# Kernel tuning notes

Measured on AMD Instinct MI355X. Metric: run time of the kernel, lower is better.

## Reference

```python
import jax, jax.numpy as jnp
import numpy as np

B = 256
VERTS_PER_MESH = 5850
V = B * VERTS_PER_MESH
E = 3 * V
NEG_SLOPE = 0.01  # nn.LeakyReLU default


def setup_inputs() -> dict:
    key = jax.random.key(0)
    ks = jax.random.split(key, 10)
    inp = {
        "verts": jax.random.normal(ks[0], (V, 3), dtype=jnp.float32),
        "edges": jax.random.randint(ks[1], (E, 2), 0, V, dtype=jnp.int64)
        if jax.config.jax_enable_x64 else jax.random.randint(ks[1], (E, 2), 0, V, dtype=jnp.int32),
        # GraphConv 1: 3 -> 5 (pytorch3d init='normal': weights ~ N(0, 0.01), bias 0)
        "w0a": jax.random.normal(ks[2], (5, 3), dtype=jnp.float32) * 0.01,
        "b0a": jnp.zeros((5,), dtype=jnp.float32),
        "w1a": jax.random.normal(ks[3], (5, 3), dtype=jnp.float32) * 0.01,
        "b1a": jnp.zeros((5,), dtype=jnp.float32),
        # GraphConv 2: 5 -> 20
        "w0b": jax.random.normal(ks[4], (20, 5), dtype=jnp.float32) * 0.01,
        "b0b": jnp.zeros((20,), dtype=jnp.float32),
        "w1b": jax.random.normal(ks[5], (20, 5), dtype=jnp.float32) * 0.01,
        "b1b": jnp.zeros((20,), dtype=jnp.float32),
        # MLP head
        "fc1_w": jax.random.normal(ks[6], (10, 20), dtype=jnp.float32) * 0.1,
        "fc1_b": jnp.zeros((10,), dtype=jnp.float32),
        "fc2_w": jax.random.normal(ks[7], (64, VERTS_PER_MESH * 10), dtype=jnp.float32) * 0.004,
        "fc2_b": jnp.zeros((64,), dtype=jnp.float32),
    }
    return inp


def graph_conv(x, edges, w0, b0, w1, b1):
    # pytorch3d GraphConv, directed=False:
    # out[v] = W0 x_v + b0 + sum_{(i,j) in edges, v in {i,j}} (W1 x_other + b1)
    out = x @ w0.T + b0                      # [V, out_dim]
    nbr = x @ w1.T + b1                      # [V, out_dim]
    i, j = edges[:, 0], edges[:, 1]
    out = out.at[i].add(nbr[j])              # scatter-add, forward direction
    out = out.at[j].add(nbr[i])              # reverse direction (undirected)
    return out


def reference(verts, edges, w0a, b0a, w1a, b1a, w0b, b0b, w1b, b1b,
              fc1_w, fc1_b, fc2_w, fc2_b):
    leaky = lambda t: jnp.where(t >= 0, t, NEG_SLOPE * t)
    x = leaky(graph_conv(verts, edges, w0a, b0a, w1a, b1a))   # [V, 5]
    x = leaky(graph_conv(x, edges, w0b, b0b, w1b, b1b))       # [V, 20]
    x = x.reshape(B, VERTS_PER_MESH, 20)                      # split/stack per mesh
    x = leaky(x @ fc1_w.T + fc1_b)                            # [B, 5850, 10]
    x = x.reshape(B, VERTS_PER_MESH * 10)                     # flatten
    x = x @ fc2_w.T + fc2_b                                   # [B, 64]
    return jax.nn.softmax(x, axis=1)
```

## Files before the change

kernel.cpp:

```cpp
#include <hip/hip_runtime.h>
#include <hip/hip_bf16.h>

#define B_MESH 256
#define VPM    5850
#define NV     (B_MESH * VPM)
#define NE     (3 * NV)
#define NDIR   (2 * NE)
#define KDIM   (VPM * 10)
#define KP     58528
#define KSPLIT 64
#define SLOPE  0.01f

#define NBK    512
#define BSZ    2925
#define NSC    4
#define CHSZ   (NV / NSC)
#define NKEY   (NBK * NSC)
#define CAPG   5320
#define PB     256
#define PTH    1024
#define PEPB   (NE / PB)
#define E4PB   (PEPB / 2)
#define NEP    ((E4PB + PTH - 1) / PTH)
#define CAPL   12
#define TRASHE ((unsigned)BSZ << 19)
#define ATH    512

#define NVB    (NV / 256)
#define W2N    (64 * KP)
#define W2BB   (W2N / 256)
#define PADN   (B_MESH * (KP - KDIM))
#define PADB   (PADN / 256)
#define RT     16

#define LBIAS 4096
#define LMASK 0x7FFFFull
#define S5A   32.f
#define B5A   125
#define S5B   16.f
#define B5B   63
#define CLAMP5 3.9f

typedef short s8v  __attribute__((ext_vector_type(8)));
typedef float f4v  __attribute__((ext_vector_type(4)));

static __device__ __forceinline__ __hip_bfloat16 f2b(float f) { return __float2bfloat16(f); }
static __device__ __forceinline__ float leaky(float x) { return x >= 0.f ? x : SLOPE * x; }

static __device__ __forceinline__ unsigned long long pack3(float a, float b, float c,
                                                           float S, float clampv)
{
    int ia = __float2int_rn(fminf(fmaxf(a, -clampv), clampv) * S) + LBIAS;
    int ib = __float2int_rn(fminf(fmaxf(b, -clampv), clampv) * S) + LBIAS;
    int ic = __float2int_rn(fminf(fmaxf(c, -clampv), clampv) * S) + LBIAS;
    return (unsigned long long)(unsigned)ia
         | ((unsigned long long)(unsigned)ib << 19)
         | ((unsigned long long)(unsigned)ic << 38)
         | (1ull << 57);
}

static __device__ __forceinline__ void unpack3(unsigned long long p, float invS,
                                               float* o0, float* o1, float* o2, int* cnt)
{
    int c  = (int)(p >> 57);
    int l0 = (int)(p & LMASK);
    int l1 = (int)((p >> 19) & LMASK);
    int l2 = (int)((p >> 38) & LMASK);
    *o0 = (float)(l0 - c * LBIAS) * invS;
    *o1 = (float)(l1 - c * LBIAS) * invS;
    *o2 = (float)(l2 - c * LBIAS) * invS;
    *cnt = c;
}

static __device__ __forceinline__ unsigned long long pack5(const float* x)
{
    unsigned long long p = 0;
#pragma unroll
    for (int c = 0; c < 4; c++) {
        int l = __float2int_rn(fminf(fmaxf(x[c], -CLAMP5), CLAMP5) * S5A) + B5A;
        p |= (unsigned long long)(unsigned)l << (13 * c);
    }
    int l4 = __float2int_rn(fminf(fmaxf(x[4], -CLAMP5), CLAMP5) * S5B) + B5B;
    p |= (unsigned long long)(unsigned)l4 << 52;
    return p;
}

static __device__ __forceinline__ void unpack5(unsigned long long p, int deg, float* o)
{
    const float invA = 1.f / S5A, invB = 1.f / S5B;
#pragma unroll
    for (int c = 0; c < 4; c++) {
        int l = (int)((p >> (13 * c)) & 0x1FFF);
        o[c] = (float)(l - deg * B5A) * invA;
    }
    int l4 = (int)(p >> 52);
    o[4] = (float)(l4 - deg * B5B) * invB;
}

__global__ void initK(const float* __restrict__ verts,
                      unsigned long long* __restrict__ vq,
                      const float* __restrict__ W2,
                      __hip_bfloat16* __restrict__ W2b,
                      unsigned* __restrict__ gcur)
{
    int blk = blockIdx.x;
    if (blk < NVB) {
        int t = blk * 256 + threadIdx.x;
        float x0 = verts[3 * t + 0], x1 = verts[3 * t + 1], x2 = verts[3 * t + 2];
        vq[t] = pack3(x0, x1, x2, 512.f, 7.9f);
    } else if (blk < NVB + W2BB) {
        int idx = (blk - NVB) * 256 + threadIdx.x;
        int n = idx / KP;
        int k = idx - n * KP;
        W2b[idx] = f2b(k < KDIM ? W2[(size_t)n * KDIM + k] : 0.f);
    } else {
        int idx = (blk - NVB - W2BB) * 256 + threadIdx.x;
        if (idx < NKEY) gcur[idx] = 0u;
    }
}

__global__ void __launch_bounds__(PTH) partK(const int4* __restrict__ edges4,
                                             unsigned* __restrict__ gcur,
                                             unsigned* __restrict__ csr)
{
    __shared__ unsigned buf[NKEY * CAPL];
    __shared__ unsigned lcur[NKEY];

    int blk = blockIdx.x, t = threadIdx.x;
#pragma unroll
    for (int r = 0; r < NKEY / PTH; r++) lcur[t + r * PTH] = 0u;
    __syncthreads();

    long q0 = (long)blk * E4PB;
    for (int ep = 0; ep < NEP; ep++) {
        int qi = ep * PTH + t;
        if (qi < E4PB) {
            int4 ee = edges4[q0 + qi];
#pragma unroll
            for (int h = 0; h < 2; h++) {
                unsigned ui = (unsigned)(h ? ee.z : ee.x);
                unsigned uj = (unsigned)(h ? ee.w : ee.y);
                unsigned dbi = ui / BSZ, dbj = uj / BSZ;
                unsigned sci = ui / CHSZ, scj = uj / CHSZ;
                unsigned k1 = dbi * NSC + scj;
                unsigned n1 = ((ui - dbi * BSZ) << 19) | (uj - scj * CHSZ);
                unsigned k2 = dbj * NSC + sci;
                unsigned n2 = ((uj - dbj * BSZ) << 19) | (ui - sci * CHSZ);
#pragma unroll
                for (int d = 0; d < 2; d++) {
                    unsigned k = d ? k2 : k1;
                    unsigned n = d ? n2 : n1;
                    unsigned p = atomicAdd(&lcur[k], 1u);
                    if (p < CAPL) buf[k * CAPL + p] = n;
                    else {
                        unsigned gb = atomicAdd(&gcur[k], 8u);
                        if (gb + 8 <= CAPG) {
                            uint4 a = {n, TRASHE, TRASHE, TRASHE};
                            uint4 b = {TRASHE, TRASHE, TRASHE, TRASHE};
                            uint4* dst = (uint4*)&csr[(size_t)k * CAPG + gb];
                            dst[0] = a; dst[1] = b;
                        }
                    }
                }
            }
        }
        __syncthreads();
#pragma unroll
        for (int r = 0; r < NKEY / PTH; r++) {
            int k = t + r * PTH;
            unsigned fill = min(lcur[k], (unsigned)CAPL);
            if (fill >= 8u) {
                unsigned gb = atomicAdd(&gcur[k], 8u);
                if (gb + 8 <= CAPG) {
                    unsigned* p = &buf[k * CAPL];
                    uint4 a = {p[0], p[1], p[2], p[3]};
                    uint4 b = {p[4], p[5], p[6], p[7]};
                    uint4* dst = (uint4*)&csr[(size_t)k * CAPG + gb];
                    dst[0] = a; dst[1] = b;
                }
                unsigned rem = fill - 8u;
                for (unsigned i = 0; i < rem; i++)
                    buf[k * CAPL + i] = buf[k * CAPL + 8 + i];
                lcur[k] = rem;
            } else lcur[k] = fill;
        }
        __syncthreads();
    }
#pragma unroll
    for (int r = 0; r < NKEY / PTH; r++) {
        int k = t + r * PTH;
        unsigned fill = min(lcur[k], (unsigned)CAPL);
        if (fill) {
            unsigned ng = (fill + 3u) >> 2;
            unsigned gb = atomicAdd(&gcur[k], ng * 4u);
            for (unsigned g = 0; g < ng; g++) {
                if (gb + (g + 1) * 4 <= CAPG) {
                    unsigned w4[4];
#pragma unroll
                    for (int i2 = 0; i2 < 4; i2++) {
                        unsigned s = g * 4 + (unsigned)i2;
                        w4[i2] = (s < fill) ? buf[k * CAPL + s] : TRASHE;
                    }
                    uint4 a = {w4[0], w4[1], w4[2], w4[3]};
                    *(uint4*)&csr[(size_t)k * CAPG + gb + g * 4] = a;
                }
            }
        }
    }
}

template<int PASS>
__global__ void __launch_bounds__(ATH) accK(const unsigned* __restrict__ csr,
                                            const unsigned* __restrict__ gcur,
                                            const unsigned long long* __restrict__ vals,
                                            const float* __restrict__ verts,
                                            const float* __restrict__ w0,
                                            const float* __restrict__ b0,
                                            const float* __restrict__ w1,
                                            const float* __restrict__ b1,
                                            unsigned long long* __restrict__ x5qOut,
                                            unsigned char* __restrict__ deg8,
                                            unsigned long long* __restrict__ R)
{
    __shared__ unsigned long long acc[BSZ + 1];
    int db = blockIdx.x, t = threadIdx.x;
    for (int i = t; i <= BSZ; i += ATH) acc[i] = 0ull;
    __syncthreads();
#pragma unroll
    for (int sc = 0; sc < NSC; sc++) {
        int key = db * NSC + sc;
        const unsigned* p = csr + (size_t)key * CAPG;
        int cnt = (int)min(gcur[key], (unsigned)CAPG);
        const unsigned long long* vb = vals + (size_t)sc * CHSZ;
        int i = t;
        for (; i + ATH < cnt; i += 2 * ATH) {
            unsigned e0 = __builtin_nontemporal_load(p + i);
            unsigned e1 = __builtin_nontemporal_load(p + i + ATH);
            unsigned long long v0 = vb[e0 & 0x7FFFFu];
            unsigned long long v1 = vb[e1 & 0x7FFFFu];
            atomicAdd(&acc[min(e0 >> 19, (unsigned)BSZ)], v0);
            atomicAdd(&acc[min(e1 >> 19, (unsigned)BSZ)], v1);
        }
        for (; i < cnt; i += ATH) {
            unsigned e = __builtin_nontemporal_load(p + i);
            atomicAdd(&acc[min(e >> 19, (unsigned)BSZ)], vb[e & 0x7FFFFu]);
        }
    }
    __syncthreads();
    int vbase = db * BSZ;
    if constexpr (PASS == 0) {
        for (int k = t; k < BSZ; k += ATH) {
            int v = vbase + k;
            float x0 = verts[3 * v + 0], x1 = verts[3 * v + 1], x2 = verts[3 * v + 2];
            float sm0, sm1, sm2; int deg;
            unpack3(acc[k], 1.f / 512.f, &sm0, &sm1, &sm2, &deg);
            deg8[v] = (unsigned char)deg;
            float dg = (float)deg;
            float x5[5];
#pragma unroll
            for (int o = 0; o < 5; o++) {
                float a = b0[o] + dg * b1[o]
                        + x0 * w0[o * 3 + 0] + x1 * w0[o * 3 + 1] + x2 * w0[o * 3 + 2]
                        + sm0 * w1[o * 3 + 0] + sm1 * w1[o * 3 + 1] + sm2 * w1[o * 3 + 2];
                x5[o] = leaky(a);
            }
            x5qOut[v] = pack5(x5);
        }
    } else {
        for (int k = t; k < BSZ; k += ATH) R[vbase + k] = acc[k];
    }
}

__global__ void convBfc1(const unsigned long long* __restrict__ x5q,
                         const unsigned long long* __restrict__ R,
                         const unsigned char* __restrict__ deg8,
                         const float* __restrict__ w0, const float* __restrict__ b0,
                         const float* __restrict__ w1, const float* __restrict__ b1,
                         const float* __restrict__ fw, const float* __restrict__ fb,
                         __hip_bfloat16* __restrict__ X10)
{
    int blk = blockIdx.x;
    if (blk >= NVB) {
        int j = (blk - NVB) * 256 + threadIdx.x;
        int row = j / (KP - KDIM);
        int c   = j - row * (KP - KDIM);
        X10[(size_t)row * KP + KDIM + c] = f2b(0.f);
        return;
    }
    int v = blk * 256 + threadIdx.x;
    int deg = (int)deg8[v];
    float xc[5], sc[5];
    unpack5(x5q[v], 1, xc);
    unpack5(R[v], deg, sc);
    float dg = (float)deg;
    float x20[20];
#pragma unroll
    for (int o = 0; o < 20; o++) {
        float a = b0[o] + dg * b1[o];
#pragma unroll
        for (int c = 0; c < 5; c++) a += xc[c] * w0[o * 5 + c] + sc[c] * w1[o * 5 + c];
        x20[o] = leaky(a);
    }
    int row = v / VPM;
    int vi  = v - row * VPM;
    __hip_bfloat16* dst = X10 + (size_t)row * KP + vi * 10;
#pragma unroll
    for (int o2 = 0; o2 < 10; o2++) {
        float a = fb[o2];
#pragma unroll
        for (int o = 0; o < 20; o++) a += x20[o] * fw[o2 * 20 + o];
        dst[o2] = f2b(leaky(a));
    }
}

__global__ void gemmMFMA(const __hip_bfloat16* __restrict__ X10,
                         const __hip_bfloat16* __restrict__ W2b,
                         float* __restrict__ part)
{
    int rt = blockIdx.x;
    int kc = blockIdx.y;
    int w    = threadIdx.x >> 6;
    int lane = threadIdx.x & 63;
    int quad = lane >> 4;
    int ml   = lane & 15;
    int s0  = kc * 28 + min(kc, 37);
    int len = 28 + (kc < 37 ? 1 : 0);

    const s8v* ap = (const s8v*)(X10 + (size_t)(rt * 16 + ml) * KP + s0 * 32 + quad * 8);
    const s8v* bp = (const s8v*)(W2b + (size_t)(w * 16 + ml) * KP + s0 * 32 + quad * 8);

    f4v c0 = {0.f, 0.f, 0.f, 0.f};
    for (int s = 0; s < len; s++) {
        s8v a = ap[s * 4];
        s8v b = bp[s * 4];
        c0 = __builtin_amdgcn_mfma_f32_16x16x32_bf16(a, b, c0, 0, 0, 0);
    }
    float* pbase = part + ((size_t)kc * B_MESH + rt * 16) * 64;
#pragma unroll
    for (int r = 0; r < 4; r++)
        pbase[(quad * 4 + r) * 64 + w * 16 + ml] = c0[r];
}

__global__ void reduceSoftmax(const float* __restrict__ part,
                              const float* __restrict__ fb2,
                              float* __restrict__ out)
{
    __shared__ float red[4][64];
    int b = blockIdx.x;
    int t = threadIdx.x;
    int n = t & 63, wq = t >> 6;
    float acc = 0.f;
#pragma unroll
    for (int q = 0; q < KSPLIT / 4; q++) {
        int p = wq + q * 4;
        acc += part[((size_t)p * B_MESH + b) * 64 + n];
    }
    red[wq][n] = acc;
    __syncthreads();
    if (wq == 0) {
        float v = fb2[n] + red[0][n] + red[1][n] + red[2][n] + red[3][n];
        float m = v;
#pragma unroll
        for (int off = 32; off; off >>= 1) m = fmaxf(m, __shfl_xor(m, off, 64));
        float e = __expf(v - m);
        float s = e;
#pragma unroll
        for (int off = 32; off; off >>= 1) s += __shfl_xor(s, off, 64);
        out[b * 64 + n] = e / s;
    }
}

extern "C" void kernel_launch(void* const* d_in, const int* in_sizes, int n_in,
                              void* d_out, int out_size, void* d_ws, size_t ws_size,
                              hipStream_t stream)
{
    const float* verts = (const float*)d_in[0];
    const int*   edges = (const int*)d_in[1];
    const float* w0a   = (const float*)d_in[2];
    const float* b0a   = (const float*)d_in[3];
    const float* w1a   = (const float*)d_in[4];
    const float* b1a   = (const float*)d_in[5];
    const float* w0b   = (const float*)d_in[6];
    const float* b0b   = (const float*)d_in[7];
    const float* w1b   = (const float*)d_in[8];
    const float* b1b   = (const float*)d_in[9];
    const float* fc1w  = (const float*)d_in[10];
    const float* fc1b  = (const float*)d_in[11];
    const float* fc2w  = (const float*)d_in[12];
    const float* fc2b  = (const float*)d_in[13];

    const size_t SZ_CSR = (size_t)NKEY * CAPG * 4;
    const size_t SZ_GC  = 8192;
    const size_t SZ_VQ  = (size_t)NV * 8;
    const size_t SZ_X5  = (size_t)NV * 8;
    const size_t SZ_R   = (size_t)NV * 8;
    const size_t SZ_W2B = (size_t)64 * KP * 2;

    char* ws = (char*)d_ws;
    unsigned*           csr  = (unsigned*)(ws);
    __hip_bfloat16*     X10  = (__hip_bfloat16*)(ws);
    unsigned*           gcur = (unsigned*)(ws + SZ_CSR);
    unsigned long long* vq   = (unsigned long long*)(ws + SZ_CSR + SZ_GC);
    unsigned long long* x5q  = (unsigned long long*)(ws + SZ_CSR + SZ_GC + SZ_VQ);
    unsigned long long* R    = (unsigned long long*)(ws + SZ_CSR + SZ_GC + SZ_VQ + SZ_X5);
    __hip_bfloat16*     W2b  = (__hip_bfloat16*)(ws + SZ_CSR + SZ_GC + SZ_VQ + SZ_X5 + SZ_R);
    unsigned char*      deg8 = (unsigned char*)(ws + SZ_CSR + SZ_GC + SZ_VQ + SZ_X5 + SZ_R + SZ_W2B);
    float*              part = (float*)R;

    initK<<<NVB + W2BB + 8, 256, 0, stream>>>(verts, vq, fc2w, W2b, gcur);
    partK<<<PB, PTH, 0, stream>>>((const int4*)edges, gcur, csr);
    accK<0><<<NBK, ATH, 0, stream>>>(csr, gcur, vq, verts, w0a, b0a, w1a, b1a,
                                     x5q, deg8, (unsigned long long*)nullptr);
    accK<1><<<NBK, ATH, 0, stream>>>(csr, gcur, x5q, verts, w0a, b0a, w1a, b1a,
                                     (unsigned long long*)nullptr, deg8, R);
    convBfc1<<<NVB + PADB, 256, 0, stream>>>(x5q, R, deg8, w0b, b0b, w1b, b1b,
                                             fc1w, fc1b, X10);
    gemmMFMA<<<dim3(RT, KSPLIT), 256, 0, stream>>>(X10, W2b, part);
    reduceSoftmax<<<B_MESH, 256, 0, stream>>>(part, fc2b, (float*)d_out);
}
```

Measured before the change: 349.3 us.

## Fuse second graph-conv epilogue and fc1 into the aggregation kernel

```diff
diff --git a/kernel.cpp b/kernel.cpp
--- a/kernel.cpp
+++ b/kernel.cpp
@@ -30,6 +30,7 @@
 #define W2N    (64 * KP)
 #define W2BB   (W2N / 256)
 #define PADN   (B_MESH * (KP - KDIM))
+#define PADBF  (PADN / ATH)
 #define PADB   (PADN / 256)
 #define RT     16
 
@@ -209,7 +210,7 @@
     }
 }
 
-template<int PASS>
+template<int PASS, int FUSED>
 __global__ void __launch_bounds__(ATH) accK(const unsigned* __restrict__ csr,
                                             const unsigned* __restrict__ gcur,
                                             const unsigned long long* __restrict__ vals,
@@ -218,12 +219,22 @@
                                             const float* __restrict__ b0,
                                             const float* __restrict__ w1,
                                             const float* __restrict__ b1,
-                                            unsigned long long* __restrict__ x5qOut,
+                                            const float* __restrict__ fw,
+                                            const float* __restrict__ fb,
+                                            unsigned long long* __restrict__ x5q,
                                             unsigned char* __restrict__ deg8,
-                                            unsigned long long* __restrict__ R)
-{
+                                            unsigned long long* __restrict__ R,
+                                            __hip_bfloat16* __restrict__ X10)
+{
+    int db = blockIdx.x, t = threadIdx.x;
+    if (PASS == 1 && FUSED && db >= NBK) {
+        int j = (db - NBK) * ATH + t;
+        int row = j / (KP - KDIM);
+        int c   = j - row * (KP - KDIM);
+        X10[(size_t)row * KP + KDIM + c] = f2b(0.f);
+        return;
+    }
     __shared__ unsigned long long acc[BSZ + 1];
-    int db = blockIdx.x, t = threadIdx.x;
     for (int i = t; i <= BSZ; i += ATH) acc[i] = 0ull;
     __syncthreads();
 #pragma unroll
@@ -233,13 +244,16 @@
         int cnt = (int)min(gcur[key], (unsigned)CAPG);
         const unsigned long long* vb = vals + (size_t)sc * CHSZ;
         int i = t;
-        for (; i + ATH < cnt; i += 2 * ATH) {
+        for (; i + 2 * ATH < cnt; i += 3 * ATH) {
             unsigned e0 = __builtin_nontemporal_load(p + i);
             unsigned e1 = __builtin_nontemporal_load(p + i + ATH);
+            unsigned e2 = __builtin_nontemporal_load(p + i + 2 * ATH);
             unsigned long long v0 = vb[e0 & 0x7FFFFu];
             unsigned long long v1 = vb[e1 & 0x7FFFFu];
+            unsigned long long v2 = vb[e2 & 0x7FFFFu];
             atomicAdd(&acc[min(e0 >> 19, (unsigned)BSZ)], v0);
             atomicAdd(&acc[min(e1 >> 19, (unsigned)BSZ)], v1);
+            atomicAdd(&acc[min(e2 >> 19, (unsigned)BSZ)], v2);
         }
         for (; i < cnt; i += ATH) {
             unsigned e = __builtin_nontemporal_load(p + i);
@@ -264,10 +278,37 @@
                         + sm0 * w1[o * 3 + 0] + sm1 * w1[o * 3 + 1] + sm2 * w1[o * 3 + 2];
                 x5[o] = leaky(a);
             }
-            x5qOut[v] = pack5(x5);
-        }
+            x5q[v] = pack5(x5);
+        }
+    } else if constexpr (!FUSED) {
+        for (int k = t; k < BSZ; k += ATH) R[vbase + k] = acc[k];
     } else {
-        for (int k = t; k < BSZ; k += ATH) R[vbase + k] = acc[k];
+        for (int k = t; k < BSZ; k += ATH) {
+            int v = vbase + k;
+            int deg = (int)deg8[v];
+            float xc[5], sc5[5];
+            unpack5(x5q[v], 1, xc);
+            unpack5(acc[k], deg, sc5);
+            float dg = (float)deg;
+            float x20[20];
+#pragma unroll
+            for (int o = 0; o < 20; o++) {
+                float a = b0[o] + dg * b1[o];
+#pragma unroll
+                for (int c = 0; c < 5; c++) a += xc[c] * w0[o * 5 + c] + sc5[c] * w1[o * 5 + c];
+                x20[o] = leaky(a);
+            }
+            int row = v / VPM;
+            int vi  = v - row * VPM;
+            __hip_bfloat16* dst = X10 + (size_t)row * KP + vi * 10;
+#pragma unroll
+            for (int o2 = 0; o2 < 10; o2++) {
+                float a = fb[o2];
+#pragma unroll
+                for (int o = 0; o < 20; o++) a += x20[o] * fw[o2 * 20 + o];
+                dst[o2] = f2b(leaky(a));
+            }
+        }
     }
 }
 
@@ -391,30 +432,50 @@
 
     const size_t SZ_CSR = (size_t)NKEY * CAPG * 4;
     const size_t SZ_GC  = 8192;
+    const size_t SZ_X5  = (size_t)NV * 8;
+    const size_t SZ_W2B = (size_t)64 * KP * 2;
+    const size_t SZ_DEG = (size_t)NV;
     const size_t SZ_VQ  = (size_t)NV * 8;
-    const size_t SZ_X5  = (size_t)NV * 8;
-    const size_t SZ_R   = (size_t)NV * 8;
-    const size_t SZ_W2B = (size_t)64 * KP * 2;
+    const size_t SZ_X10 = (size_t)B_MESH * KP * 2;
+    const size_t offGC  = SZ_CSR;
+    const size_t offX5  = offGC + SZ_GC;
+    const size_t offW2B = offX5 + SZ_X5;
+    const size_t offDEG = offW2B + SZ_W2B;
+    const size_t offVQ  = offDEG + SZ_DEG;
+    const size_t needFused = offVQ + SZ_X10;
+
+    bool fused = ws_size >= needFused;
 
     char* ws = (char*)d_ws;
-    unsigned*           csr  = (unsigned*)(ws);
-    __hip_bfloat16*     X10  = (__hip_bfloat16*)(ws);
-    unsigned*           gcur = (unsigned*)(ws + SZ_CSR);
-    unsigned long long* vq   = (unsigned long long*)(ws + SZ_CSR + SZ_GC);
-    unsigned long long* x5q  = (unsigned long long*)(ws + SZ_CSR + SZ_GC + SZ_VQ);
-    unsigned long long* R    = (unsigned long long*)(ws + SZ_CSR + SZ_GC + SZ_VQ + SZ_X5);
-    __hip_bfloat16*     W2b  = (__hip_bfloat16*)(ws + SZ_CSR + SZ_GC + SZ_VQ + SZ_X5 + SZ_R);
-    unsigned char*      deg8 = (unsigned char*)(ws + SZ_CSR + SZ_GC + SZ_VQ + SZ_X5 + SZ_R + SZ_W2B);
-    float*              part = (float*)R;
+    unsigned*           csr  = (unsigned*)ws;
+    unsigned*           gcur = (unsigned*)(ws + offGC);
+    unsigned long long* x5q  = (unsigned long long*)(ws + offX5);
+    __hip_bfloat16*     W2b  = (__hip_bfloat16*)(ws + offW2B);
+    unsigned char*      deg8 = (unsigned char*)(ws + offDEG);
+    unsigned long long* vq   = (unsigned long long*)(ws + offVQ);
+    unsigned long long* R    = fused ? nullptr
+                                     : (unsigned long long*)(ws + offVQ + SZ_VQ);
+    __hip_bfloat16*     X10  = fused ? (__hip_bfloat16*)(ws + offVQ)
+                                     : (__hip_bfloat16*)ws;
+    float*              part = fused ? (float*)ws
+                                     : (float*)R;
 
     initK<<<NVB + W2BB + 8, 256, 0, stream>>>(verts, vq, fc2w, W2b, gcur);
     partK<<<PB, PTH, 0, stream>>>((const int4*)edges, gcur, csr);
-    accK<0><<<NBK, ATH, 0, stream>>>(csr, gcur, vq, verts, w0a, b0a, w1a, b1a,
-                                     x5q, deg8, (unsigned long long*)nullptr);
-    accK<1><<<NBK, ATH, 0, stream>>>(csr, gcur, x5q, verts, w0a, b0a, w1a, b1a,
-                                     (unsigned long long*)nullptr, deg8, R);
-    convBfc1<<<NVB + PADB, 256, 0, stream>>>(x5q, R, deg8, w0b, b0b, w1b, b1b,
-                                             fc1w, fc1b, X10);
+    accK<0, 0><<<NBK, ATH, 0, stream>>>(csr, gcur, vq, verts,
+                                        w0a, b0a, w1a, b1a, nullptr, nullptr,
+                                        x5q, deg8, nullptr, nullptr);
+    if (fused) {
+        accK<1, 1><<<NBK + PADBF, ATH, 0, stream>>>(csr, gcur, x5q, verts,
+                                                    w0b, b0b, w1b, b1b, fc1w, fc1b,
+                                                    x5q, deg8, nullptr, X10);
+    } else {
+        accK<1, 0><<<NBK, ATH, 0, stream>>>(csr, gcur, x5q, verts,
+                                            w0b, b0b, w1b, b1b, fc1w, fc1b,
+                                            x5q, deg8, R, nullptr);
+        convBfc1<<<NVB + PADB, 256, 0, stream>>>(x5q, R, deg8, w0b, b0b, w1b, b1b,
+                                                 fc1w, fc1b, X10);
+    }
     gemmMFMA<<<dim3(RT, KSPLIT), 256, 0, stream>>>(X10, W2b, part);
     reduceSoftmax<<<B_MESH, 256, 0, stream>>>(part, fc2b, (float*)d_out);
 }
```

Measured after the change: 387.3 us. 1.11x slower.
